# Optimization experiments

Hardware: AMD Instinct MI355X
Metric: run time of the kernel (lower is better)

## Reference

```python
import math
import jax, jax.numpy as jnp
import numpy as np

T, D, H, HD, ETA, R = 4096, 1024, 8, 64, 4, 7
EPS = 1e-5


def _discounted_sum(start_state, x, discounts):
    """state[t] = state[t-1]*discounts[t] + x[t], scanned over leading axis T."""
    def step(s, xd):
        xt, dt = xd
        s = s * dt + xt
        return s, s
    _, ys = jax.lax.scan(step, start_state, (x, discounts))
    return ys  # (T, *)


def _forward(inputs, terminations, tilde_k_prev, tilde_v_prev, s_prev, tick,
             W_kqv, b_kqv, W_p, b_p, W_proj, b_proj):
    cur_seq = inputs.shape[0]
    term = terminations.astype(inputs.dtype)

    kqv = (inputs @ W_kqv + b_kqv).reshape(cur_seq, H, 5 * HD)
    keys, queries, values, beta, gammas = jnp.split(kqv, 5, axis=-1)  # each (T,H,HD)
    p = (inputs @ W_p + b_p).reshape(cur_seq, H, 3 * ETA)
    p1, p2, p3 = jnp.split(p, 3, axis=-1)  # each (T,H,ETA)

    # feature-map expansion: outer product over (eta, head_dim) -> flatten to eta*HD
    keys = jnp.einsum('chd,chn->chnd', jax.nn.relu(keys), jax.nn.relu(p1)).reshape(cur_seq, H, ETA * HD)
    queries = jnp.einsum('chd,chn->chnd', jax.nn.relu(queries), jax.nn.relu(p2)).reshape(cur_seq, H, ETA * HD)
    gammas = jnp.einsum('chd,chn->chnd', jax.nn.sigmoid(gammas), jax.nn.sigmoid(p3)).reshape(cur_seq, H, ETA * HD)
    beta = jax.nn.sigmoid(beta)  # (T,H,HD)

    ticks = tick.reshape(1, 1) + jnp.arange(1, cur_seq + 1, dtype=inputs.dtype).reshape(-1, 1)  # (T,1)->(T,R)
    omegas = jnp.linspace(-math.pi, math.pi, R).astype(inputs.dtype).reshape(1, -1)
    occil = jnp.cos(ticks * omegas)  # (T,R)

    values = values * beta
    values = values[:, None, :, :] * occil[:, :, None, None]  # (T,R,H,HD)
    keys = keys * gammas
    s = keys  # (T,H,ETA*HD)
    keys = keys[:, None, :, :] * occil[:, :, None, None]  # (T,R,H,ETA*HD)

    not_term = (1.0 - term).reshape(cur_seq, 1, 1)
    discount_gamma = (1.0 - gammas) * not_term  # (T,H,ETA*HD)
    discount_beta = (1.0 - beta) * not_term     # (T,H,HD)

    final_keys = _discounted_sum(tilde_k_prev, keys, discount_gamma[:, None])    # (T,R,H,ETA*HD)
    final_values = _discounted_sum(tilde_v_prev, values, discount_beta[:, None])  # (T,R,H,HD)
    final_s = _discounted_sum(s_prev, s, discount_gamma)                          # (T,H,ETA*HD)

    kdq = jnp.einsum('crhd,chd->crh', final_keys, queries)
    kv = jnp.einsum('crhd,crh->chd', final_values, kdq)  # sum over r
    norm = jnp.einsum('chd,chd->ch', final_s, queries)
    attn_out = kv / (2 * R * norm[..., None] + EPS)
    attn_out = attn_out.reshape(cur_seq, H * HD) @ W_proj + b_proj  # dropout p=0.0 is identity

    new_tick = tick + cur_seq
    return attn_out, final_keys[-1], final_values[-1], final_s[-1], new_tick


def setup_inputs() -> dict:
    key = jax.random.key(0)
    ks = jax.random.split(key, 5)
    return {
        'inputs': jax.random.normal(ks[0], (T, D), jnp.float32),
        'terminations': jax.random.randint(ks[1], (T,), 0, 2, jnp.int32),
        'tilde_k_prev': jnp.zeros((R, H, ETA * HD), jnp.float32),
        'tilde_v_prev': jnp.zeros((R, H, HD), jnp.float32),
        's_prev': jnp.zeros((H, ETA * HD), jnp.float32),
        'tick': jnp.ones((1,), jnp.float32),
        'W_kqv': jax.random.normal(ks[2], (D, H * HD * 5), jnp.float32) * 0.02,
        'b_kqv': jnp.zeros((H * HD * 5,), jnp.float32),
        'W_p': jax.random.normal(ks[3], (D, H * ETA * 3), jnp.float32) * 0.02,
        'b_p': jnp.zeros((H * ETA * 3,), jnp.float32),
        'W_proj': jax.random.normal(ks[4], (H * HD, D), jnp.float32) * 0.02,
        'b_proj': jnp.zeros((D,), jnp.float32),
    }


def reference(inputs, terminations, tilde_k_prev, tilde_v_prev, s_prev, tick,
              W_kqv, b_kqv, W_p, b_p, W_proj, b_proj):
    return _forward(inputs, terminations, tilde_k_prev, tilde_v_prev, s_prev, tick,
                    W_kqv, b_kqv, W_p, b_p, W_proj, b_proj)
```

## Files before the change

### kernel.cpp

```cpp
#include <hip/hip_runtime.h>
#include <hip/hip_bf16.h>
#include <math.h>

#define T_SEQ 4096
#define DIM   1024
#define NH    8
#define HDIM  64
#define ETA   4
#define NR    7
#define NKQVC 2688
#define CHUNK 16
#define NCHUNK 256

typedef __attribute__((ext_vector_type(8))) short bf16x8;
typedef __attribute__((ext_vector_type(4))) short short4v;
typedef __attribute__((ext_vector_type(4))) float f32x4;

#define KQVC_OFF    0ul
#define OCC_OFF     5505024ul
#define BTPROJ_OFF  5537792ul
#define ATTNBF_OFF  5799936ul
#define BIASC_OFF   6848512ul
#define ABF_OFF     6851328ul
#define BTCAT_OFF   8948480ul
#define YSUM_OFF    6851328ul
#define CARRY_OFF   12618496ul

#define O_ATTN 0ul
#define O_FK   4194304ul
#define O_FV   4208640ul
#define O_FS   4212224ul
#define O_TICK 4214272ul

__device__ __forceinline__ float sigm(float x) { return 1.f / (1.f + __expf(-x)); }

__device__ __forceinline__ short f2bf(float f) {
  union { __hip_bfloat16 b; short s; } u;
  u.b = __float2bfloat16(f);
  return u.s;
}
__device__ __forceinline__ float bf2f(short s) {
  union { __hip_bfloat16 b; short s2; } u;
  u.s2 = s;
  return __bfloat162float(u.b);
}

__device__ __forceinline__ void gload16(const void* g, void* l) {
  __builtin_amdgcn_global_load_lds(
      (const __attribute__((address_space(1))) void*)g,
      (__attribute__((address_space(3))) void*)l, 16, 0, 0);
}

__global__ __launch_bounds__(256) void cast_f32_bf16(
    const float* __restrict__ x, short* __restrict__ y) {
  size_t i = (size_t)(blockIdx.x * 256 + threadIdx.x) * 4;
  float4 v = *(const float4*)(x + i);
  short4v o;
  o.x = f2bf(v.x); o.y = f2bf(v.y); o.z = f2bf(v.z); o.w = f2bf(v.w);
  *(short4v*)(y + i) = o;
}

__global__ __launch_bounds__(256) void transpose_cast(
    const float* __restrict__ W, short* __restrict__ Bt, int K, int N) {
  __shared__ float tile[32][33];
  int n0 = blockIdx.x * 32, k0 = blockIdx.y * 32;
  int tx = threadIdx.x, ty = threadIdx.y;
  for (int i = ty; i < 32; i += 8)
    tile[i][tx] = W[(size_t)(k0 + i) * N + n0 + tx];
  __syncthreads();
  for (int i = ty; i < 32; i += 8)
    Bt[(size_t)(n0 + i) * K + k0 + tx] = f2bf(tile[tx][i]);
}

__global__ __launch_bounds__(256) void concat_bias(
    const float* __restrict__ b_kqv, const float* __restrict__ b_p,
    float* __restrict__ bc) {
  int i = blockIdx.x * 256 + threadIdx.x;
  if (i >= NKQVC) return;
  bc[i] = (i < 2560) ? b_kqv[i] : (i < 2656 ? b_p[i - 2560] : 0.f);
}

template <int OUT_BF16>
__global__ __launch_bounds__(256) void gemm_bt_mfma(
    const short* __restrict__ A, const short* __restrict__ Bt,
    const float* __restrict__ bias, void* __restrict__ Cout,
    int M, int N, int K) {
  __shared__ __align__(16) short lds[16384];

  int nwg = gridDim.x;
  int cpx = nwg >> 3;
  int bid = blockIdx.x;
  int swz = (bid & 7) * cpx + (bid >> 3);
  int nbx = N >> 7;
  int bm0 = (swz / nbx) << 7;
  int bn0 = (swz % nbx) << 7;

  const int tid = threadIdx.x;
  const int w = tid >> 6, l = tid & 63;
  const int wm = w >> 1, wn = w & 1;
  const int fr = l & 15;
  const int fq = l >> 4;

  const int ca = w * 2;
  const short* Ag0 = A + (size_t)(bm0 + ca * 16 + (l >> 2)) * K + (l & 3) * 8;
  const short* Ag1 = Ag0 + (size_t)16 * K;
  const short* Bg0 = Bt + (size_t)(bn0 + ca * 16 + (l >> 2)) * K + (l & 3) * 8;
  const short* Bg1 = Bg0 + (size_t)16 * K;

  f32x4 acc[4][4];
#pragma unroll
  for (int mi = 0; mi < 4; ++mi)
#pragma unroll
    for (int ni = 0; ni < 4; ++ni)
#pragma unroll
      for (int r = 0; r < 4; ++r) acc[mi][ni][r] = 0.f;

  const int KT = K >> 5;
  int cur = 0;
  {
    short* la = &lds[ca * 512];
    short* lb = &lds[4096 + ca * 512];
    gload16(Ag0, la);
    gload16(Ag1, la + 512);
    gload16(Bg0, lb);
    gload16(Bg1, lb + 512);
  }
  __syncthreads();

  for (int kt = 0; kt < KT; ++kt) {
    if (kt + 1 < KT) {
      int nb = (cur ^ 1) * 8192;
      int ko = (kt + 1) * 32;
      short* la = &lds[nb + ca * 512];
      short* lb = &lds[nb + 4096 + ca * 512];
      gload16(Ag0 + ko, la);
      gload16(Ag1 + ko, la + 512);
      gload16(Bg0 + ko, lb);
      gload16(Bg1 + ko, lb + 512);
    }
    const short* ArP = &lds[cur * 8192 + (wm * 64 + fr) * 32 + fq * 8];
    const short* BrP = &lds[cur * 8192 + 4096 + (wn * 64 + fr) * 32 + fq * 8];
    bf16x8 af[4], bfv[4];
#pragma unroll
    for (int mi = 0; mi < 4; ++mi) af[mi] = *(const bf16x8*)(ArP + mi * 512);
#pragma unroll
    for (int ni = 0; ni < 4; ++ni) bfv[ni] = *(const bf16x8*)(BrP + ni * 512);
#pragma unroll
    for (int mi = 0; mi < 4; ++mi)
#pragma unroll
      for (int ni = 0; ni < 4; ++ni)
        acc[mi][ni] = __builtin_amdgcn_mfma_f32_16x16x32_bf16(
            af[mi], bfv[ni], acc[mi][ni], 0, 0, 0);
    __syncthreads();
    cur ^= 1;
  }

  if (OUT_BF16) {
#pragma unroll
    for (int ni = 0; ni < 4; ++ni) {
      int col = wn * 64 + ni * 16 + fr;
      float bz = bias[bn0 + col];
#pragma unroll
      for (int mi = 0; mi < 4; ++mi) {
        int row = wm * 64 + mi * 16 + fq * 4;
#pragma unroll
        for (int r = 0; r < 4; ++r)
          lds[(row + r) * 128 + col] = f2bf(acc[mi][ni][r] + bz);
      }
    }
    __syncthreads();
    int row = tid >> 1, half = tid & 1;
    const f32x4* src = (const f32x4*)&lds[row * 128 + half * 64];
    f32x4* dst = (f32x4*)((short*)Cout + (size_t)(bm0 + row) * N + bn0 + half * 64);
#pragma unroll
    for (int i = 0; i < 8; ++i) dst[i] = src[i];
  } else {
#pragma unroll
    for (int ni = 0; ni < 4; ++ni) {
      int col = bn0 + wn * 64 + ni * 16 + fr;
      float bz = bias[col];
#pragma unroll
      for (int mi = 0; mi < 4; ++mi) {
        int row = bm0 + wm * 64 + mi * 16 + fq * 4;
#pragma unroll
        for (int r = 0; r < 4; ++r)
          ((float*)Cout)[(size_t)(row + r) * N + col] = acc[mi][ni][r] + bz;
      }
    }
  }
}

__global__ __launch_bounds__(256) void occil_kernel(const float* __restrict__ tick,
                                                    float* __restrict__ occ) {
  int t = blockIdx.x * 256 + threadIdx.x;
  if (t >= T_SEQ) return;
  float tickt = tick[0] + (float)(t + 1);
#pragma unroll
  for (int r = 0; r < NR; ++r) {
    float om = (float)(-3.14159265358979323846 + r * (3.14159265358979323846 / 3.0));
    occ[t * 8 + r] = cosf(tickt * om);
  }
  occ[t * 8 + 7] = 0.f;
}

__device__ __forceinline__ void stage_gates_half(
    const short* __restrict__ kqv, const int* __restrict__ term,
    short* glA, short* glB, int c, int h, int w, int dd, int half) {
#pragma unroll
  for (int j = 0; j < 2; ++j) {
    int tt = w * 2 + j;
    int tg = c * CHUNK + half * 8 + tt;
    size_t base = (size_t)tg * NKQVC + h * 320 + dd;
    float kx = bf2f(kqv[base]);
    float qx = bf2f(kqv[base + 64]);
    float vx = bf2f(kqv[base + 128]);
    float bx = bf2f(kqv[base + 192]);
    float gx = bf2f(kqv[base + 256]);
    const short* pp = kqv + (size_t)tg * NKQVC + 2560 + h * 12;
    float nt = 1.f - (float)term[tg];
    float rk = fmaxf(kx, 0.f), rq = fmaxf(qx, 0.f);
    float sg = sigm(gx), sb = sigm(bx);
    bf16x8 oA, oB;
#pragma unroll
    for (int n = 0; n < 4; ++n) {
      float rp1 = fmaxf(bf2f(pp[n]), 0.f);
      float rp2 = fmaxf(bf2f(pp[4 + n]), 0.f);
      float sp3 = sigm(bf2f(pp[8 + n]));
      float gam = sg * sp3;
      oA[n]     = f2bf(rk * rp1 * gam);
      oA[4 + n] = f2bf((1.f - gam) * nt);
      oB[n]     = f2bf(rq * rp2);
    }
    oB[4] = f2bf(vx * sb);
    oB[5] = f2bf((1.f - sb) * nt);
    oB[6] = 0; oB[7] = 0;
    *(bf16x8*)&glA[(tt * 64 + dd) * 8] = oA;
    *(bf16x8*)&glB[(tt * 64 + dd) * 8] = oB;
  }
}

__global__ __launch_bounds__(256) void pass_a(
    const short* __restrict__ kqv, const float* __restrict__ occ,
    const int* __restrict__ term, float* __restrict__ ysum) {
  const int c = blockIdx.x, h = blockIdx.y;
  const int tid = threadIdx.x;
  const int w = tid >> 6, dd = tid & 63;
  const int R0 = w * 2;
  const int RN = (w == 3) ? 1 : 2;
  const bool w3 = (w == 3);
  __shared__ __align__(16) short glA[8 * 64 * 8];
  __shared__ __align__(16) short glB[8 * 64 * 8];
  __shared__ float socc[CHUNK][8];
  for (int i = tid; i < CHUNK * 8; i += 256)
    socc[i >> 3][i & 7] = occ[(size_t)c * CHUNK * 8 + i];

  float yk[2][ETA], yv[2], ys[ETA], Pg[ETA], Pb = 1.f;
#pragma unroll
  for (int rr = 0; rr < 2; ++rr) {
    yv[rr] = 0.f;
#pragma unroll
    for (int n = 0; n < ETA; ++n) yk[rr][n] = 0.f;
  }
#pragma unroll
  for (int n = 0; n < ETA; ++n) { ys[n] = 0.f; Pg[n] = 1.f; }

  for (int half = 0; half < 2; ++half) {
    stage_gates_half(kqv, term, glA, glB, c, h, w, dd, half);
    __syncthreads();
    for (int tt = 0; tt < 8; ++tt) {
      int t = half * 8 + tt;
      bf16x8 gA = *(const bf16x8*)&glA[(tt * 64 + dd) * 8];
      bf16x8 gB = *(const bf16x8*)&glB[(tt * 64 + dd) * 8];
      float occr[2];
#pragma unroll
      for (int rr = 0; rr < 2; ++rr)
        occr[rr] = socc[t][(R0 + rr) < 7 ? (R0 + rr) : 7];
#pragma unroll
      for (int n = 0; n < ETA; ++n) {
        float xs = bf2f(gA[n]);
        float dg = bf2f(gA[4 + n]);
        if (w3) {
          Pg[n] *= dg;
          ys[n] = fmaf(ys[n], dg, xs);
        }
#pragma unroll
        for (int rr = 0; rr < 2; ++rr)
          if (rr < RN) yk[rr][n] = fmaf(yk[rr][n], dg, xs * occr[rr]);
      }
      float vb = bf2f(gB[4]);
      float db = bf2f(gB[5]);
      if (w3) Pb *= db;
#pragma unroll
      for (int rr = 0; rr < 2; ++rr)
        if (rr < RN) yv[rr] = fmaf(yv[rr], db, vb * occr[rr]);
    }
    __syncthreads();
  }

  float* o = ysum + (size_t)(c * NH + h) * 44 * 64 + dd;
#pragma unroll
  for (int rr = 0; rr < 2; ++rr)
    if (rr < RN) {
#pragma unroll
      for (int n = 0; n < ETA; ++n) o[((R0 + rr) * 4 + n) * 64] = yk[rr][n];
      o[(28 + R0 + rr) * 64] = yv[rr];
    }
  if (w3) {
#pragma unroll
    for (int n = 0; n < ETA; ++n) o[(35 + n) * 64] = ys[n];
#pragma unroll
    for (int n = 0; n < ETA; ++n) o[(39 + n) * 64] = Pg[n];
    o[43 * 64] = Pb;
  }
}

__global__ __launch_bounds__(256) void pass_b(
    const float* __restrict__ ysum, float* __restrict__ carry,
    const float* __restrict__ k_prev, const float* __restrict__ v_prev,
    const float* __restrict__ s_prev) {
  int idx = blockIdx.x * 256 + threadIdx.x;
  int dd = idx & 63;
  int slot = (idx >> 6) % 39;
  int h = idx / (39 * 64);

  int pslot;
  float f;
  if (slot < 28) {
    int r = slot >> 2, n = slot & 3;
    f = k_prev[(size_t)(r * NH + h) * 256 + n * 64 + dd];
    pslot = 39 + n;
  } else if (slot < 35) {
    int r = slot - 28;
    f = v_prev[(size_t)(r * NH + h) * 64 + dd];
    pslot = 43;
  } else {
    int n = slot - 35;
    f = s_prev[(size_t)h * 256 + n * 64 + dd];
    pslot = 39 + n;
  }
  const size_t YSTR = (size_t)NH * 2816;
  const size_t CSTR = (size_t)NH * 2496;
  const float* yb = ysum + (size_t)h * 2816 + slot * 64 + dd;
  const float* pb = ysum + (size_t)h * 2816 + pslot * 64 + dd;
  float* cb = carry + (size_t)h * 2496 + slot * 64 + dd;

#define PD 16
  float yring[PD], pring[PD];
#pragma unroll
  for (int d = 0; d < PD; ++d) {
    yring[d] = yb[(size_t)d * YSTR];
    pring[d] = pb[(size_t)d * YSTR];
  }
  const int NB = NCHUNK / PD;
  for (int cb2 = 0; cb2 < NB; ++cb2) {
    int c0 = cb2 * PD;
    float ynext[PD], pnext[PD];
    if (cb2 + 1 < NB) {
#pragma unroll
      for (int j = 0; j < PD; ++j) {
        ynext[j] = yb[(size_t)(c0 + PD + j) * YSTR];
        pnext[j] = pb[(size_t)(c0 + PD + j) * YSTR];
      }
    }
#pragma unroll
    for (int j = 0; j < PD; ++j) {
      cb[(size_t)(c0 + j) * CSTR] = f;
      f = fmaf(f, pring[j], yring[j]);
    }
    if (cb2 + 1 < NB) {
#pragma unroll
      for (int j = 0; j < PD; ++j) { yring[j] = ynext[j]; pring[j] = pnext[j]; }
    }
  }
#undef PD
}

__global__ __launch_bounds__(256) void pass_c(
    const short* __restrict__ kqv, const float* __restrict__ occ,
    const int* __restrict__ term, const float* __restrict__ carry,
    short* __restrict__ attn, float* __restrict__ out,
    const float* __restrict__ tick) {
  const int c = blockIdx.x, h = blockIdx.y;
  const int tid = threadIdx.x;
  const int w = tid >> 6, dd = tid & 63;
  const int R0 = w * 2;
  const int RN = (w == 3) ? 1 : 2;
  const bool w3 = (w == 3);
  __shared__ __align__(16) short glA[8 * 64 * 8];
  __shared__ __align__(16) short glB[8 * 64 * 8];
  __shared__ float socc[CHUNK][8];
  __shared__ float xch[5][8][64];
  for (int i = tid; i < CHUNK * 8; i += 256)
    socc[i >> 3][i & 7] = occ[(size_t)c * CHUNK * 8 + i];

  const float* cp = carry + (size_t)(c * NH + h) * 2496 + dd;
  float fk[2][ETA], fv[2], fs[ETA];
#pragma unroll
  for (int rr = 0; rr < 2; ++rr)
    if (rr < RN) {
#pragma unroll
      for (int n = 0; n < ETA; ++n) fk[rr][n] = cp[((R0 + rr) * 4 + n) * 64];
      fv[rr] = cp[(28 + R0 + rr) * 64];
    }
  if (w3) {
#pragma unroll
    for (int n = 0; n < ETA; ++n) fs[n] = cp[(35 + n) * 64];
  }

  for (int half = 0; half < 2; ++half) {
    stage_gates_half(kqv, term, glA, glB, c, h, w, dd, half);
    __syncthreads();
    for (int tt = 0; tt < 8; ++tt) {
      int t = half * 8 + tt;
      bf16x8 gA = *(const bf16x8*)&glA[(tt * 64 + dd) * 8];
      bf16x8 gB = *(const bf16x8*)&glB[(tt * 64 + dd) * 8];
      float occr[2];
#pragma unroll
      for (int rr = 0; rr < 2; ++rr)
        occr[rr] = socc[t][(R0 + rr) < 7 ? (R0 + rr) : 7];
      float kdqp[2] = {0.f, 0.f};
      float normp = 0.f;
#pragma unroll
      for (int n = 0; n < ETA; ++n) {
        float xs = bf2f(gA[n]);
        float dg = bf2f(gA[4 + n]);
        float qf = bf2f(gB[n]);
        if (w3) {
          fs[n] = fmaf(fs[n], dg, xs);
          normp = fmaf(fs[n], qf, normp);
        }
#pragma unroll
        for (int rr = 0; rr < 2; ++rr)
          if (rr < RN) {
            fk[rr][n] = fmaf(fk[rr][n], dg, xs * occr[rr]);
            kdqp[rr]  = fmaf(fk[rr][n], qf, kdqp[rr]);
          }
      }
      float vb = bf2f(gB[4]);
      float db = bf2f(gB[5]);
#pragma unroll
      for (int rr = 0; rr < 2; ++rr)
        if (rr < RN) fv[rr] = fmaf(fv[rr], db, vb * occr[rr]);

      float red[2];
      red[0] = kdqp[0];
      red[1] = w3 ? normp : kdqp[1];
#pragma unroll
      for (int i = 0; i < 2; ++i) {
        float x = red[i];
#pragma unroll
        for (int m = 1; m < 64; m <<= 1) x += __shfl_xor(x, m, 64);
        red[i] = x;
      }
      float kvvP = fv[0] * red[0];
      if (!w3) kvvP = fmaf(fv[1], red[1], kvvP);
      xch[w][tt][dd] = kvvP;
      if (w3) xch[4][tt][dd] = fmaf(14.f, red[1], 1e-5f);
    }
    __syncthreads();
#pragma unroll
    for (int j = 0; j < 2; ++j) {
      int tt = w * 2 + j;
      int t = half * 8 + tt;
      float kvv = xch[0][tt][dd] + xch[1][tt][dd] + xch[2][tt][dd] + xch[3][tt][dd];
      attn[(size_t)(c * CHUNK + t) * 512 + h * 64 + dd] = f2bf(kvv / xch[4][tt][dd]);
    }
  }

  if (c == NCHUNK - 1) {
#pragma unroll
    for (int rr = 0; rr < 2; ++rr)
      if (rr < RN) {
#pragma unroll
        for (int n = 0; n < ETA; ++n)
          out[O_FK + (size_t)((R0 + rr) * NH + h) * 256 + n * 64 + dd] = fk[rr][n];
        out[O_FV + (size_t)((R0 + rr) * NH + h) * 64 + dd] = fv[rr];
      }
    if (w3) {
#pragma unroll
      for (int n = 0; n < ETA; ++n)
        out[O_FS + (size_t)h * 256 + n * 64 + dd] = fs[n];
    }
    if (w == 0 && h == 0 && dd == 0) out[O_TICK] = tick[0] + (float)T_SEQ;
  }
}

extern "C" void kernel_launch(void* const* d_in, const int* in_sizes, int n_in,
                              void* d_out, int out_size, void* d_ws, size_t ws_size,
                              hipStream_t stream) {
  const float* inputs = (const float*)d_in[0];
  const int*   term   = (const int*)d_in[1];
  const float* k_prev = (const float*)d_in[2];
  const float* v_prev = (const float*)d_in[3];
  const float* s_prev = (const float*)d_in[4];
  const float* tick   = (const float*)d_in[5];
  const float* W_kqv  = (const float*)d_in[6];
  const float* b_kqv  = (const float*)d_in[7];
  const float* W_p    = (const float*)d_in[8];
  const float* b_p    = (const float*)d_in[9];
  const float* W_proj = (const float*)d_in[10];
  const float* b_proj = (const float*)d_in[11];
  float* out = (float*)d_out;
  float* ws  = (float*)d_ws;

  short* kqvc   = (short*)(ws + KQVC_OFF);
  float* occ    = ws + OCC_OFF;
  short* BtProj = (short*)(ws + BTPROJ_OFF);
  short* attnbf = (short*)(ws + ATTNBF_OFF);
  float* biasc  = ws + BIASC_OFF;
  short* Abf    = (short*)(ws + ABF_OFF);
  short* BtCat  = (short*)(ws + BTCAT_OFF);
  float* ysum   = ws + YSUM_OFF;
  float* carry  = ws + CARRY_OFF;

  cast_f32_bf16<<<4096, 256, 0, stream>>>(inputs, Abf);
  transpose_cast<<<dim3(80, 32), dim3(32, 8), 0, stream>>>(W_kqv, BtCat, 1024, 2560);
  transpose_cast<<<dim3(3, 32), dim3(32, 8), 0, stream>>>(
      W_p, BtCat + (size_t)2560 * 1024, 1024, 96);
  transpose_cast<<<dim3(32, 16), dim3(32, 8), 0, stream>>>(W_proj, BtProj, 512, 1024);
  concat_bias<<<11, 256, 0, stream>>>(b_kqv, b_p, biasc);

  occil_kernel<<<16, 256, 0, stream>>>(tick, occ);

  gemm_bt_mfma<1><<<672, 256, 0, stream>>>(Abf, BtCat, biasc, kqvc,
                                           T_SEQ, NKQVC, DIM);

  pass_a<<<dim3(NCHUNK, NH), 256, 0, stream>>>(kqvc, occ, term, ysum);
  pass_b<<<78, 256, 0, stream>>>(ysum, carry, k_prev, v_prev, s_prev);
  pass_c<<<dim3(NCHUNK, NH), 256, 0, stream>>>(kqvc, occ, term, carry,
                                               attnbf, out, tick);

  gemm_bt_mfma<0><<<256, 256, 0, stream>>>(attnbf, BtProj, b_proj, out,
                                           T_SEQ, DIM, NH * HDIM);
}
```

Before: 145.3 us.

## Triple-buffer GEMM LDS loads with partial vmcnt waits

Moves the MFMA GEMM main loop from double to triple buffering in LDS, prefetching two k-tiles ahead. Barriers are preceded by s_waitcnt vmcnt(4), so only the older tile must land before the barrier and the newest loads stay in flight across it. This is meant to hide global load latency better. LDS use grows from 32KB to 48KB per block, which may reduce occupancy. The manual waitcnt also depends on gload16 issuing exactly one vm op per call.

```diff
diff --git a/kernel.cpp b/kernel.cpp
--- a/kernel.cpp
+++ b/kernel.cpp
@@ -85,7 +85,7 @@
     const short* __restrict__ A, const short* __restrict__ Bt,
     const float* __restrict__ bias, void* __restrict__ Cout,
     int M, int N, int K) {
-  __shared__ __align__(16) short lds[16384];
+  __shared__ __align__(16) short lds[3 * 8192];
 
   int nwg = gridDim.x;
   int cpx = nwg >> 3;
@@ -116,28 +116,27 @@
       for (int r = 0; r < 4; ++r) acc[mi][ni][r] = 0.f;
 
   const int KT = K >> 5;
+
+#define STAGE(buf, ko)                                   \
+  do {                                                   \
+    short* la_ = &lds[(buf) * 8192 + ca * 512];          \
+    short* lb_ = &lds[(buf) * 8192 + 4096 + ca * 512];   \
+    gload16(Ag0 + (ko), la_);                            \
+    gload16(Ag1 + (ko), la_ + 512);                      \
+    gload16(Bg0 + (ko), lb_);                            \
+    gload16(Bg1 + (ko), lb_ + 512);                      \
+  } while (0)
+
+  STAGE(0, 0);
+  STAGE(1, 32);
+  asm volatile("s_waitcnt vmcnt(4)" ::: "memory");
+  __builtin_amdgcn_s_barrier();
+
   int cur = 0;
-  {
-    short* la = &lds[ca * 512];
-    short* lb = &lds[4096 + ca * 512];
-    gload16(Ag0, la);
-    gload16(Ag1, la + 512);
-    gload16(Bg0, lb);
-    gload16(Bg1, lb + 512);
-  }
-  __syncthreads();
-
   for (int kt = 0; kt < KT; ++kt) {
-    if (kt + 1 < KT) {
-      int nb = (cur ^ 1) * 8192;
-      int ko = (kt + 1) * 32;
-      short* la = &lds[nb + ca * 512];
-      short* lb = &lds[nb + 4096 + ca * 512];
-      gload16(Ag0 + ko, la);
-      gload16(Ag1 + ko, la + 512);
-      gload16(Bg0 + ko, lb);
-      gload16(Bg1 + ko, lb + 512);
-    }
+    int nxt = cur + 2; if (nxt >= 3) nxt -= 3;
+    if (kt + 2 < KT) STAGE(nxt, (kt + 2) * 32);
+
     const short* ArP = &lds[cur * 8192 + (wm * 64 + fr) * 32 + fq * 8];
     const short* BrP = &lds[cur * 8192 + 4096 + (wn * 64 + fr) * 32 + fq * 8];
     bf16x8 af[4], bfv[4];
@@ -151,9 +150,15 @@
       for (int ni = 0; ni < 4; ++ni)
         acc[mi][ni] = __builtin_amdgcn_mfma_f32_16x16x32_bf16(
             af[mi], bfv[ni], acc[mi][ni], 0, 0, 0);
-    __syncthreads();
-    cur ^= 1;
-  }
+
+    if (kt + 2 < KT)
+      asm volatile("s_waitcnt vmcnt(4)" ::: "memory");
+    else
+      asm volatile("s_waitcnt vmcnt(0)" ::: "memory");
+    __builtin_amdgcn_s_barrier();
+    cur = (cur + 1 == 3) ? 0 : cur + 1;
+  }
+#undef STAGE
 
   if (OUT_BF16) {
 #pragma unroll
```

Measured after the change: 146.5 us. No clear change (+0.9%).

## Fuse prologue kernels into one launch and store scan partials in bf16

Applied to the files above, without the earlier changes.

Six small preprocessing kernels (input cast, three weight transposes, bias concat, oscillator table) are merged into a single block-indexed prologue launch to cut launch overhead. The chunk-scan intermediate sums and carries passed between pass_a, pass_b and pass_c are now stored as bf16 instead of fp32, halving that traffic. The carry buffer offset moves to fit the smaller layout. Storing the carried recurrence states and decay products in bf16 loses precision and may hurt accuracy over long scans.

```diff
diff --git a/kernel.cpp b/kernel.cpp
--- a/kernel.cpp
+++ b/kernel.cpp
@@ -24,7 +24,7 @@
 #define ABF_OFF     6851328ul
 #define BTCAT_OFF   8948480ul
 #define YSUM_OFF    6851328ul
-#define CARRY_OFF   12618496ul
+#define CARRY_OFF   9734912ul
 
 #define O_ATTN 0ul
 #define O_FK   4194304ul
@@ -51,33 +51,63 @@
       (__attribute__((address_space(3))) void*)l, 16, 0, 0);
 }
 
-__global__ __launch_bounds__(256) void cast_f32_bf16(
-    const float* __restrict__ x, short* __restrict__ y) {
-  size_t i = (size_t)(blockIdx.x * 256 + threadIdx.x) * 4;
-  float4 v = *(const float4*)(x + i);
-  short4v o;
-  o.x = f2bf(v.x); o.y = f2bf(v.y); o.z = f2bf(v.z); o.w = f2bf(v.w);
-  *(short4v*)(y + i) = o;
-}
-
-__global__ __launch_bounds__(256) void transpose_cast(
-    const float* __restrict__ W, short* __restrict__ Bt, int K, int N) {
+__global__ __launch_bounds__(256) void prologue(
+    const float* __restrict__ inputs, short* __restrict__ Abf,
+    const float* __restrict__ W_kqv, const float* __restrict__ W_p,
+    const float* __restrict__ W_proj, short* __restrict__ BtCat,
+    short* __restrict__ BtProj, const float* __restrict__ b_kqv,
+    const float* __restrict__ b_p, float* __restrict__ biasc,
+    const float* __restrict__ tick, float* __restrict__ occ) {
+  const int b = blockIdx.x;
+  const int tid = threadIdx.x;
   __shared__ float tile[32][33];
-  int n0 = blockIdx.x * 32, k0 = blockIdx.y * 32;
-  int tx = threadIdx.x, ty = threadIdx.y;
-  for (int i = ty; i < 32; i += 8)
-    tile[i][tx] = W[(size_t)(k0 + i) * N + n0 + tx];
-  __syncthreads();
-  for (int i = ty; i < 32; i += 8)
-    Bt[(size_t)(n0 + i) * K + k0 + tx] = f2bf(tile[tx][i]);
-}
-
-__global__ __launch_bounds__(256) void concat_bias(
-    const float* __restrict__ b_kqv, const float* __restrict__ b_p,
-    float* __restrict__ bc) {
-  int i = blockIdx.x * 256 + threadIdx.x;
-  if (i >= NKQVC) return;
-  bc[i] = (i < 2560) ? b_kqv[i] : (i < 2656 ? b_p[i - 2560] : 0.f);
+  const int tx = tid & 31, ty = tid >> 5;
+
+  if (b < 4096) {
+    size_t i = ((size_t)b * 256 + tid) * 4;
+    float4 v = *(const float4*)(inputs + i);
+    short4v o;
+    o.x = f2bf(v.x); o.y = f2bf(v.y); o.z = f2bf(v.z); o.w = f2bf(v.w);
+    *(short4v*)(Abf + i) = o;
+  } else if (b < 6656) {
+    int blk = b - 4096;
+    int n0 = (blk % 80) * 32, k0 = (blk / 80) * 32;
+    for (int i = ty; i < 32; i += 8)
+      tile[i][tx] = W_kqv[(size_t)(k0 + i) * 2560 + n0 + tx];
+    __syncthreads();
+    for (int i = ty; i < 32; i += 8)
+      BtCat[(size_t)(n0 + i) * 1024 + k0 + tx] = f2bf(tile[tx][i]);
+  } else if (b < 6752) {
+    int blk = b - 6656;
+    int n0 = (blk % 3) * 32, k0 = (blk / 3) * 32;
+    for (int i = ty; i < 32; i += 8)
+      tile[i][tx] = W_p[(size_t)(k0 + i) * 96 + n0 + tx];
+    __syncthreads();
+    short* dst = BtCat + (size_t)2560 * 1024;
+    for (int i = ty; i < 32; i += 8)
+      dst[(size_t)(n0 + i) * 1024 + k0 + tx] = f2bf(tile[tx][i]);
+  } else if (b < 7264) {
+    int blk = b - 6752;
+    int n0 = (blk % 32) * 32, k0 = (blk / 32) * 32;
+    for (int i = ty; i < 32; i += 8)
+      tile[i][tx] = W_proj[(size_t)(k0 + i) * 1024 + n0 + tx];
+    __syncthreads();
+    for (int i = ty; i < 32; i += 8)
+      BtProj[(size_t)(n0 + i) * 512 + k0 + tx] = f2bf(tile[tx][i]);
+  } else if (b < 7275) {
+    int i = (b - 7264) * 256 + tid;
+    if (i < NKQVC)
+      biasc[i] = (i < 2560) ? b_kqv[i] : (i < 2656 ? b_p[i - 2560] : 0.f);
+  } else {
+    int t = (b - 7275) * 256 + tid;
+    float tickt = tick[0] + (float)(t + 1);
+#pragma unroll
+    for (int r = 0; r < NR; ++r) {
+      float om = (float)(-3.14159265358979323846 + r * (3.14159265358979323846 / 3.0));
+      occ[t * 8 + r] = cosf(tickt * om);
+    }
+    occ[t * 8 + 7] = 0.f;
+  }
 }
 
 template <int OUT_BF16>
@@ -188,19 +218,6 @@
       }
     }
   }
-}
-
-__global__ __launch_bounds__(256) void occil_kernel(const float* __restrict__ tick,
-                                                    float* __restrict__ occ) {
-  int t = blockIdx.x * 256 + threadIdx.x;
-  if (t >= T_SEQ) return;
-  float tickt = tick[0] + (float)(t + 1);
-#pragma unroll
-  for (int r = 0; r < NR; ++r) {
-    float om = (float)(-3.14159265358979323846 + r * (3.14159265358979323846 / 3.0));
-    occ[t * 8 + r] = cosf(tickt * om);
-  }
-  occ[t * 8 + 7] = 0.f;
 }
 
 __device__ __forceinline__ void stage_gates_half(
@@ -241,7 +258,7 @@
 
 __global__ __launch_bounds__(256) void pass_a(
     const short* __restrict__ kqv, const float* __restrict__ occ,
-    const int* __restrict__ term, float* __restrict__ ysum) {
+    const int* __restrict__ term, short* __restrict__ ysum) {
   const int c = blockIdx.x, h = blockIdx.y;
   const int tid = threadIdx.x;
   const int w = tid >> 6, dd = tid & 63;
@@ -297,25 +314,25 @@
     __syncthreads();
   }
 
-  float* o = ysum + (size_t)(c * NH + h) * 44 * 64 + dd;
+  short* o = ysum + (size_t)(c * NH + h) * 44 * 64 + dd;
 #pragma unroll
   for (int rr = 0; rr < 2; ++rr)
     if (rr < RN) {
 #pragma unroll
-      for (int n = 0; n < ETA; ++n) o[((R0 + rr) * 4 + n) * 64] = yk[rr][n];
-      o[(28 + R0 + rr) * 64] = yv[rr];
+      for (int n = 0; n < ETA; ++n) o[((R0 + rr) * 4 + n) * 64] = f2bf(yk[rr][n]);
+      o[(28 + R0 + rr) * 64] = f2bf(yv[rr]);
     }
   if (w3) {
 #pragma unroll
-    for (int n = 0; n < ETA; ++n) o[(35 + n) * 64] = ys[n];
-#pragma unroll
-    for (int n = 0; n < ETA; ++n) o[(39 + n) * 64] = Pg[n];
-    o[43 * 64] = Pb;
+    for (int n = 0; n < ETA; ++n) o[(35 + n) * 64] = f2bf(ys[n]);
+#pragma unroll
+    for (int n = 0; n < ETA; ++n) o[(39 + n) * 64] = f2bf(Pg[n]);
+    o[43 * 64] = f2bf(Pb);
   }
 }
 
 __global__ __launch_bounds__(256) void pass_b(
-    const float* __restrict__ ysum, float* __restrict__ carry,
+    const short* __restrict__ ysum, short* __restrict__ carry,
     const float* __restrict__ k_prev, const float* __restrict__ v_prev,
     const float* __restrict__ s_prev) {
   int idx = blockIdx.x * 256 + threadIdx.x;
@@ -340,16 +357,16 @@
   }
   const size_t YSTR = (size_t)NH * 2816;
   const size_t CSTR = (size_t)NH * 2496;
-  const float* yb = ysum + (size_t)h * 2816 + slot * 64 + dd;
-  const float* pb = ysum + (size_t)h * 2816 + pslot * 64 + dd;
-  float* cb = carry + (size_t)h * 2496 + slot * 64 + dd;
+  const short* yb = ysum + (size_t)h * 2816 + slot * 64 + dd;
+  const short* pb = ysum + (size_t)h * 2816 + pslot * 64 + dd;
+  short* cb = carry + (size_t)h * 2496 + slot * 64 + dd;
 
 #define PD 16
   float yring[PD], pring[PD];
 #pragma unroll
   for (int d = 0; d < PD; ++d) {
-    yring[d] = yb[(size_t)d * YSTR];
-    pring[d] = pb[(size_t)d * YSTR];
+    yring[d] = bf2f(yb[(size_t)d * YSTR]);
+    pring[d] = bf2f(pb[(size_t)d * YSTR]);
   }
   const int NB = NCHUNK / PD;
   for (int cb2 = 0; cb2 < NB; ++cb2) {
@@ -358,13 +375,13 @@
     if (cb2 + 1 < NB) {
 #pragma unroll
       for (int j = 0; j < PD; ++j) {
-        ynext[j] = yb[(size_t)(c0 + PD + j) * YSTR];
-        pnext[j] = pb[(size_t)(c0 + PD + j) * YSTR];
+        ynext[j] = bf2f(yb[(size_t)(c0 + PD + j) * YSTR]);
+        pnext[j] = bf2f(pb[(size_t)(c0 + PD + j) * YSTR]);
       }
     }
 #pragma unroll
     for (int j = 0; j < PD; ++j) {
-      cb[(size_t)(c0 + j) * CSTR] = f;
+      cb[(size_t)(c0 + j) * CSTR] = f2bf(f);
       f = fmaf(f, pring[j], yring[j]);
     }
     if (cb2 + 1 < NB) {
@@ -377,7 +394,7 @@
 
 __global__ __launch_bounds__(256) void pass_c(
     const short* __restrict__ kqv, const float* __restrict__ occ,
-    const int* __restrict__ term, const float* __restrict__ carry,
+    const int* __restrict__ term, const short* __restrict__ carry,
     short* __restrict__ attn, float* __restrict__ out,
     const float* __restrict__ tick) {
   const int c = blockIdx.x, h = blockIdx.y;
@@ -393,18 +410,18 @@
   for (int i = tid; i < CHUNK * 8; i += 256)
     socc[i >> 3][i & 7] = occ[(size_t)c * CHUNK * 8 + i];
 
-  const float* cp = carry + (size_t)(c * NH + h) * 2496 + dd;
+  const short* cp = carry + (size_t)(c * NH + h) * 2496 + dd;
   float fk[2][ETA], fv[2], fs[ETA];
 #pragma unroll
   for (int rr = 0; rr < 2; ++rr)
     if (rr < RN) {
 #pragma unroll
-      for (int n = 0; n < ETA; ++n) fk[rr][n] = cp[((R0 + rr) * 4 + n) * 64];
-      fv[rr] = cp[(28 + R0 + rr) * 64];
+      for (int n = 0; n < ETA; ++n) fk[rr][n] = bf2f(cp[((R0 + rr) * 4 + n) * 64]);
+      fv[rr] = bf2f(cp[(28 + R0 + rr) * 64]);
     }
   if (w3) {
 #pragma unroll
-    for (int n = 0; n < ETA; ++n) fs[n] = cp[(35 + n) * 64];
+    for (int n = 0; n < ETA; ++n) fs[n] = bf2f(cp[(35 + n) * 64]);
   }
 
   for (int half = 0; half < 2; ++half) {
@@ -510,17 +527,12 @@
   float* biasc  = ws + BIASC_OFF;
   short* Abf    = (short*)(ws + ABF_OFF);
   short* BtCat  = (short*)(ws + BTCAT_OFF);
-  float* ysum   = ws + YSUM_OFF;
-  float* carry  = ws + CARRY_OFF;
-
-  cast_f32_bf16<<<4096, 256, 0, stream>>>(inputs, Abf);
-  transpose_cast<<<dim3(80, 32), dim3(32, 8), 0, stream>>>(W_kqv, BtCat, 1024, 2560);
-  transpose_cast<<<dim3(3, 32), dim3(32, 8), 0, stream>>>(
-      W_p, BtCat + (size_t)2560 * 1024, 1024, 96);
-  transpose_cast<<<dim3(32, 16), dim3(32, 8), 0, stream>>>(W_proj, BtProj, 512, 1024);
-  concat_bias<<<11, 256, 0, stream>>>(b_kqv, b_p, biasc);
-
-  occil_kernel<<<16, 256, 0, stream>>>(tick, occ);
+  short* ysum   = (short*)(ws + YSUM_OFF);
+  short* carry  = (short*)(ws + CARRY_OFF);
+
+  prologue<<<7291, 256, 0, stream>>>(inputs, Abf, W_kqv, W_p, W_proj,
+                                     BtCat, BtProj, b_kqv, b_p, biasc,
+                                     tick, occ);
 
   gemm_bt_mfma<1><<<672, 256, 0, stream>>>(Abf, BtCat, biasc, kqvc,
                                            T_SEQ, NKQVC, DIM);
```

Measured after the change: 129.9 us, median of 2. 1.12x faster.
